# Kernel tuning notes

Hardware: AMD Instinct MI355X
Metric: run time of the kernel (lower is better)

## Reference

```python
import jax, jax.numpy as jnp
import numpy as np

NUM_HEADS = 8
EPS = 1e-3

N_TOKENS = 32768
DIM = 256
N_WIN = 128
WIN = N_TOKENS // N_WIN  # 256 tokens per window


def setup_inputs() -> dict:
    key = jax.random.key(0)
    ks = jax.random.split(key, 4)
    x = jax.random.normal(ks[0], (N_TOKENS, DIM), dtype=jnp.float32)
    # torch nn.Linear weights are [out_features, in_features]
    w_qkv = jax.random.normal(ks[1], (3 * DIM, DIM), dtype=jnp.float32) * (DIM ** -0.5)
    w_proj = jax.random.normal(ks[2], (DIM, DIM), dtype=jnp.float32) * (DIM ** -0.5)
    b_proj = jnp.zeros((DIM,), dtype=jnp.float32)
    batch_win_inds = (jnp.arange(N_TOKENS) // WIN).astype(jnp.int64)
    offsets = (jnp.arange(N_WIN) * WIN).astype(jnp.int64)
    counts = jnp.full((N_WIN,), WIN, dtype=jnp.int64)
    return {"x": x, "w_qkv": w_qkv, "w_proj": w_proj, "b_proj": b_proj,
            "offsets": offsets, "counts": counts, "batch_win_inds": batch_win_inds}


def reference(x, w_qkv, w_proj, b_proj, offsets, counts, batch_win_inds):
    N, C = x.shape
    H = NUM_HEADS
    hd = C // H
    W = counts.shape[0]  # number of windows (static)

    qkv = x @ w_qkv.T                      # [N, 3C]
    q, k, v = jnp.split(qkv, 3, axis=-1)   # each [N, C]
    q = jax.nn.relu(q.reshape(N, H, hd))   # [N, H, hd]
    k = jax.nn.relu(k.reshape(N, H, hd))
    v = v.reshape(N, H, hd)

    seg = batch_win_inds.astype(jnp.int32)
    # per-window KV state: kv[w] = sum_{i in w} k_i^T v_i   -> [W, H, hd, hd]
    kv = jax.ops.segment_sum(jnp.einsum('nhc,nhd->nhcd', k, v), seg, num_segments=W)
    # per-window key sum for normalizer                      -> [W, H, hd]
    s = jax.ops.segment_sum(k, seg, num_segments=W)

    y = jnp.einsum('nhc,nhcd->nhd', q, kv[seg])              # [N, H, hd]
    z = jnp.sum(s[seg] * q, axis=-1, keepdims=True)          # [N, H, 1]
    y = y / (z + EPS)

    y = y.reshape(N, C) @ w_proj.T + b_proj                  # [N, C]
    return y
```

## Files before the change

kernel.cpp:

```cpp
#include <hip/hip_runtime.h>

typedef __bf16 bf16_t;
typedef bf16_t bf16x8 __attribute__((ext_vector_type(8)));
typedef bf16_t bf16x4 __attribute__((ext_vector_type(4)));
typedef float f32x4 __attribute__((ext_vector_type(4)));

#define M_TOK 32768
#define NWIN 128
#define WIN  256

typedef __attribute__((address_space(3))) void* as3p;
typedef const __attribute__((address_space(1))) void* as1p;

__device__ __forceinline__ void gll16(const void* g, void* l) {
    __builtin_amdgcn_global_load_lds((as1p)g, (as3p)l, 16, 0, 0);
}

__device__ __forceinline__ bf16x8 cvt8(f32x4 a, f32x4 b) {
    bf16x8 o;
    o[0] = (bf16_t)a[0]; o[1] = (bf16_t)a[1]; o[2] = (bf16_t)a[2]; o[3] = (bf16_t)a[3];
    o[4] = (bf16_t)b[0]; o[5] = (bf16_t)b[1]; o[6] = (bf16_t)b[2]; o[7] = (bf16_t)b[3];
    return o;
}

#define VMW_(n) asm volatile("s_waitcnt vmcnt(" #n ")" ::: "memory")
#define VMW(n) VMW_(n)

__global__ __launch_bounds__(256) void wconv(
    const float* __restrict__ wq, const float* __restrict__ wp,
    bf16_t* __restrict__ wqb, bf16_t* __restrict__ wpb)
{
    int i4 = (blockIdx.x * 256 + threadIdx.x) * 4;
    const float* s; bf16_t* dst; int idx;
    if (i4 < 196608) { s = wq; dst = wqb; idx = i4; }
    else             { s = wp; dst = wpb; idx = i4 - 196608; }
    f32x4 v = *(const f32x4*)(s + idx);
    bf16x4 o;
    o[0] = (bf16_t)v[0]; o[1] = (bf16_t)v[1]; o[2] = (bf16_t)v[2]; o[3] = (bf16_t)v[3];
    *(bf16x4*)(dst + idx) = o;
}

__global__ __launch_bounds__(256) void gemm1_qkv(
    const float* __restrict__ X,
    const bf16_t* __restrict__ Wb,
    bf16_t* __restrict__ QKV)
{
    __shared__ __align__(16) float  As[3][128][32];
    __shared__ __align__(16) bf16_t Bs[3][128][32];

    const int tid = threadIdx.x;
    const int lane = tid & 63;
    const int wv = tid >> 6;
    const int wm = wv >> 1, wn = wv & 1;
    const int id = blockIdx.x;
    const int sg = id / 48, wsub = id % 48;
    const int m0 = (sg * 8 + (wsub & 7)) * 128;
    const int n0 = (wsub >> 3) * 128;
    const int r = lane & 15, q = lane >> 4;
    const int arow = lane >> 3;
    const int ag = (lane & 7) ^ arow;
    const int brow = lane >> 2;
    const int bg = (lane & 3) ^ (brow & 3);

    f32x4 acc[4][4] = {};

    auto stage = [&](int t, int buf) {
        const int kc = t * 32;
#pragma unroll
        for (int u = 0; u < 4; ++u) {
            const int rb = wv * 32 + u * 8;
            gll16(X + (size_t)(m0 + rb + arow) * 256 + kc + ag * 4, &As[buf][rb][0]);
        }
#pragma unroll
        for (int u = 0; u < 2; ++u) {
            const int rb = wv * 32 + u * 16;
            gll16(Wb + (size_t)(n0 + rb + brow) * 256 + kc + bg * 8, &Bs[buf][rb][0]);
        }
    };
    auto compute = [&](int buf) {
        bf16x8 a[4], b[4];
#pragma unroll
        for (int i = 0; i < 4; ++i) {
            const int row = wm * 64 + i * 16 + r;
            const int g0 = (2 * q) ^ (r & 7);
            const int g1 = (2 * q + 1) ^ (r & 7);
            f32x4 lo = *(const f32x4*)&As[buf][row][g0 * 4];
            f32x4 hi = *(const f32x4*)&As[buf][row][g1 * 4];
            a[i] = cvt8(lo, hi);
        }
#pragma unroll
        for (int j = 0; j < 4; ++j)
            b[j] = *(const bf16x8*)&Bs[buf][wn * 64 + j * 16 + r][(q ^ (r & 3)) * 8];
#pragma unroll
        for (int i = 0; i < 4; ++i)
#pragma unroll
            for (int j = 0; j < 4; ++j)
                acc[i][j] = __builtin_amdgcn_mfma_f32_16x16x32_bf16(b[j], a[i], acc[i][j], 0, 0, 0);
    };

    stage(0, 0); stage(1, 1); stage(2, 2);

#define G1_STEP(t, NW) do { \
        VMW(NW); \
        __builtin_amdgcn_s_barrier(); \
        __builtin_amdgcn_sched_barrier(0); \
        compute((t) % 3); \
        __builtin_amdgcn_sched_barrier(0); \
        __builtin_amdgcn_s_barrier(); \
        if ((t) + 3 < 8) stage((t) + 3, (t) % 3); \
    } while (0)

    G1_STEP(0, 12); G1_STEP(1, 12); G1_STEP(2, 12); G1_STEP(3, 12);
    G1_STEP(4, 12); G1_STEP(5, 12); G1_STEP(6, 6);  G1_STEP(7, 0);
#undef G1_STEP

#pragma unroll
    for (int i = 0; i < 4; ++i) {
        const int rowg = m0 + wm * 64 + i * 16 + r;
#pragma unroll
        for (int j = 0; j < 4; ++j) {
            const int nb = n0 + wn * 64 + j * 16 + q * 4;
            const int nblk = nb >> 5, d = nb & 31;
            bf16x4 o;
#pragma unroll
            for (int reg = 0; reg < 4; ++reg) {
                float v = acc[i][j][reg];
                if (nblk < 16) v = fmaxf(v, 0.0f);
                o[reg] = (bf16_t)v;
            }
            *(bf16x4*)&QKV[((size_t)nblk * M_TOK + rowg) * 32 + d] = o;
        }
    }
}

__global__ __launch_bounds__(256) void gemm2_proj(
    const bf16_t* __restrict__ Y,
    const bf16_t* __restrict__ Wb,
    const float* __restrict__ bias,
    float* __restrict__ Out)
{
    __shared__ __align__(16) bf16_t As[3][128][32];
    __shared__ __align__(16) bf16_t Bs[3][64][32];

    const int tid = threadIdx.x;
    const int lane = tid & 63;
    const int wv = tid >> 6;
    const int wm = wv >> 1, wn = wv & 1;
    const int id = blockIdx.x;
    const int sg = id / 32, wsub = id % 32;
    const int m0 = (sg * 8 + (wsub & 7)) * 128;
    const int n0 = (wsub >> 3) * 64;
    const int r = lane & 15, q = lane >> 4;
    const int brow = lane >> 2;
    const int bg = (lane & 3) ^ (brow & 3);

    f32x4 acc[4][2] = {};

    auto stage = [&](int t, int buf) {
        const int kc = t * 32;
#pragma unroll
        for (int u = 0; u < 2; ++u) {
            const int rb = wv * 32 + u * 16;
            gll16(Y + (size_t)(m0 + rb + brow) * 256 + kc + bg * 8, &As[buf][rb][0]);
        }
        gll16(Wb + (size_t)(n0 + wv * 16 + brow) * 256 + kc + bg * 8, &Bs[buf][wv * 16][0]);
    };
    auto compute = [&](int buf) {
        bf16x8 a[4], b[2];
#pragma unroll
        for (int i = 0; i < 4; ++i)
            a[i] = *(const bf16x8*)&As[buf][wm * 64 + i * 16 + r][(q ^ (r & 3)) * 8];
#pragma unroll
        for (int j = 0; j < 2; ++j)
            b[j] = *(const bf16x8*)&Bs[buf][wn * 32 + j * 16 + r][(q ^ (r & 3)) * 8];
#pragma unroll
        for (int i = 0; i < 4; ++i)
#pragma unroll
            for (int j = 0; j < 2; ++j)
                acc[i][j] = __builtin_amdgcn_mfma_f32_16x16x32_bf16(b[j], a[i], acc[i][j], 0, 0, 0);
    };

    stage(0, 0); stage(1, 1); stage(2, 2);

#define G2_STEP(t, NW) do { \
        VMW(NW); \
        __builtin_amdgcn_s_barrier(); \
        __builtin_amdgcn_sched_barrier(0); \
        compute((t) % 3); \
        __builtin_amdgcn_sched_barrier(0); \
        __builtin_amdgcn_s_barrier(); \
        if ((t) + 3 < 8) stage((t) + 3, (t) % 3); \
    } while (0)

    G2_STEP(0, 6); G2_STEP(1, 6); G2_STEP(2, 6); G2_STEP(3, 6);
    G2_STEP(4, 6); G2_STEP(5, 6); G2_STEP(6, 3); G2_STEP(7, 0);
#undef G2_STEP

#pragma unroll
    for (int i = 0; i < 4; ++i) {
        const int rowg = m0 + wm * 64 + i * 16 + r;
#pragma unroll
        for (int j = 0; j < 2; ++j) {
            const int nb = n0 + wn * 32 + j * 16 + q * 4;
            f32x4 bi = *(const f32x4*)(bias + nb);
            f32x4 o;
#pragma unroll
            for (int reg = 0; reg < 4; ++reg) o[reg] = acc[i][j][reg] + bi[reg];
            *(f32x4*)&Out[(size_t)rowg * 256 + nb] = o;
        }
    }
}

__global__ __launch_bounds__(256) void kvy_kernel(
    const bf16_t* __restrict__ QKV,
    const int* __restrict__ offsets,
    const int* __restrict__ counts,
    bf16_t* __restrict__ Y)
{
    const int w = blockIdx.x;
    const int h = blockIdx.y;
    const int is64 = (counts[1] == 0) ? 1 : 0;
    const int off = offsets[w << is64];
    const int tid = threadIdx.x;
    const int lane = tid & 63;
    const int wv = tid >> 6;

    __shared__ __align__(16) bf16_t KT[32 * 264];
    __shared__ __align__(16) bf16_t VT[32 * 264];
    __shared__ __align__(16) bf16_t KVT[32 * 40];
    __shared__ float sbuf[32];
    __shared__ float spart[32 * 8];
    __shared__ float zinv[WIN];

    {
        const int t = tid;
        const bf16_t* kp = QKV + ((size_t)(8 + h) * M_TOK + off + t) * 32;
        const bf16_t* vp = QKV + ((size_t)(16 + h) * M_TOK + off + t) * 32;
        bf16_t ka[32], va[32];
#pragma unroll
        for (int u = 0; u < 4; ++u) {
            bf16x8 kk = *(const bf16x8*)(kp + u * 8);
            bf16x8 vvv = *(const bf16x8*)(vp + u * 8);
#pragma unroll
            for (int j = 0; j < 8; ++j) { ka[u * 8 + j] = kk[j]; va[u * 8 + j] = vvv[j]; }
        }
#pragma unroll
        for (int c = 0; c < 32; ++c) {
            KT[c * 264 + t] = ka[c];
            VT[c * 264 + t] = va[c];
        }
    }
    __syncthreads();

    {
        const int c = tid >> 3;
        const int tc = (tid & 7) * 32;
        float ps = 0.f;
#pragma unroll
        for (int u = 0; u < 4; ++u) {
            bf16x8 kk = *(const bf16x8*)(&KT[c * 264 + tc + u * 8]);
#pragma unroll
            for (int j = 0; j < 8; ++j) ps += (float)kk[j];
        }
        spart[c * 8 + (tid & 7)] = ps;
    }
    {
        const int i = wv >> 1, j = wv & 1;
        const int r = lane & 15, q = lane >> 4;
        f32x4 acc = {};
#pragma unroll
        for (int ch = 0; ch < 8; ++ch) {
            bf16x8 af = *(const bf16x8*)(&KT[(i * 16 + r) * 264 + ch * 32 + q * 8]);
            bf16x8 bf_ = *(const bf16x8*)(&VT[(j * 16 + r) * 264 + ch * 32 + q * 8]);
            acc = __builtin_amdgcn_mfma_f32_16x16x32_bf16(af, bf_, acc, 0, 0, 0);
        }
        bf16x4 kv4;
#pragma unroll
        for (int reg = 0; reg < 4; ++reg) kv4[reg] = (bf16_t)acc[reg];
        *(bf16x4*)(&KVT[(j * 16 + r) * 40 + i * 16 + q * 4]) = kv4;
    }
    __syncthreads();
    if (tid < 32) {
        float s = 0.f;
#pragma unroll
        for (int u = 0; u < 8; ++u) s += spart[tid * 8 + u];
        sbuf[tid] = s;
    }
    __syncthreads();

    {
        const int t = tid;
        const bf16_t* qp = QKV + ((size_t)h * M_TOK + off + t) * 32;
        float z = 0.f;
#pragma unroll
        for (int u = 0; u < 4; ++u) {
            bf16x8 qq = *(const bf16x8*)(qp + u * 8);
#pragma unroll
            for (int j = 0; j < 8; ++j) z += (float)qq[j] * sbuf[u * 8 + j];
        }
        zinv[t] = 1.0f / (z + 1e-3f);
    }
    __syncthreads();

    {
        const int r = lane & 15, q = lane >> 4;
        bf16x8 b0 = *(const bf16x8*)(&KVT[(r) * 40 + q * 8]);
        bf16x8 b1 = *(const bf16x8*)(&KVT[(16 + r) * 40 + q * 8]);
#pragma unroll
        for (int u = 0; u < 4; ++u) {
            const int mi = wv * 4 + u;
            const bf16_t* ap = QKV + ((size_t)h * M_TOK + off + mi * 16 + r) * 32 + q * 8;
            bf16x8 af = *(const bf16x8*)ap;
            f32x4 acc0 = {}, acc1 = {};
            acc0 = __builtin_amdgcn_mfma_f32_16x16x32_bf16(b0, af, acc0, 0, 0, 0);
            acc1 = __builtin_amdgcn_mfma_f32_16x16x32_bf16(b1, af, acc1, 0, 0, 0);
            const int tkn = mi * 16 + r;
            const float zi = zinv[tkn];
            bf16_t* yp = Y + (size_t)(off + tkn) * 256 + h * 32;
            bf16x4 o0, o1;
#pragma unroll
            for (int reg = 0; reg < 4; ++reg) {
                o0[reg] = (bf16_t)(acc0[reg] * zi);
                o1[reg] = (bf16_t)(acc1[reg] * zi);
            }
            *(bf16x4*)(yp + q * 4) = o0;
            *(bf16x4*)(yp + 16 + q * 4) = o1;
        }
    }
}

extern "C" void kernel_launch(void* const* d_in, const int* in_sizes, int n_in,
                              void* d_out, int out_size, void* d_ws, size_t ws_size,
                              hipStream_t stream) {
    const float* x      = (const float*)d_in[0];
    const float* w_qkv  = (const float*)d_in[1];
    const float* w_proj = (const float*)d_in[2];
    const float* b_proj = (const float*)d_in[3];
    const int*   offs   = (const int*)d_in[4];
    const int*   cnts   = (const int*)d_in[5];

    char* ws = (char*)d_ws;
    bf16_t* QKV = (bf16_t*)ws;
    bf16_t* Y   = (bf16_t*)(ws + 50331648);
    bf16_t* Wqb = (bf16_t*)(ws + 67108864);
    bf16_t* Wpb = (bf16_t*)(ws + 67502080);
    float*  out = (float*)d_out;

    wconv<<<256, 256, 0, stream>>>(w_qkv, w_proj, Wqb, Wpb);

    gemm1_qkv<<<1536, 256, 0, stream>>>(x, Wqb, QKV);

    kvy_kernel<<<dim3(NWIN, 8), 256, 0, stream>>>(QKV, offs, cnts, Y);

    gemm2_proj<<<1024, 256, 0, stream>>>(Y, Wpb, b_proj, out);
}
```

Baseline: 145.4 us.

## Keep full-K A row block resident in LDS and sweep all N tiles per block

Both GEMMs now give each 512-thread block a 128-row slab of A that is loaded once into LDS in bf16 (converted from fp32 in gemm1, copied directly in gemm2). The block then loops over all output column tiles, streaming weight tiles through a triple buffer. This removes the repeated reads of X that the old grid made, once per N-tile, and the repeated per-tile fp32 to bf16 conversion. The cost is a much smaller grid of 256 blocks, lower occupancy from the large LDS footprint, and a serial initial A load that is not overlapped with compute in gemm1.

```diff
diff --git a/kernel.cpp b/kernel.cpp
--- a/kernel.cpp
+++ b/kernel.cpp
@@ -40,175 +40,197 @@
     *(bf16x4*)(dst + idx) = o;
 }
 
-__global__ __launch_bounds__(256) void gemm1_qkv(
+__global__ __launch_bounds__(512) void gemm1_qkv(
     const float* __restrict__ X,
     const bf16_t* __restrict__ Wb,
     bf16_t* __restrict__ QKV)
 {
-    __shared__ __align__(16) float  As[3][128][32];
-    __shared__ __align__(16) bf16_t Bs[3][128][32];
+    __shared__ __align__(16) bf16_t Al[128][256];
+    __shared__ __align__(16) bf16_t Bs[3][128][64];
 
     const int tid = threadIdx.x;
     const int lane = tid & 63;
     const int wv = tid >> 6;
-    const int wm = wv >> 1, wn = wv & 1;
-    const int id = blockIdx.x;
-    const int sg = id / 48, wsub = id % 48;
-    const int m0 = (sg * 8 + (wsub & 7)) * 128;
-    const int n0 = (wsub >> 3) * 128;
+    const int wm = wv >> 2, wn = wv & 3;
+    const int m0 = blockIdx.x * 128;
     const int r = lane & 15, q = lane >> 4;
-    const int arow = lane >> 3;
-    const int ag = (lane & 7) ^ arow;
-    const int brow = lane >> 2;
-    const int bg = (lane & 3) ^ (brow & 3);
-
-    f32x4 acc[4][4] = {};
-
-    auto stage = [&](int t, int buf) {
-        const int kc = t * 32;
-#pragma unroll
-        for (int u = 0; u < 4; ++u) {
-            const int rb = wv * 32 + u * 8;
-            gll16(X + (size_t)(m0 + rb + arow) * 256 + kc + ag * 4, &As[buf][rb][0]);
-        }
-#pragma unroll
-        for (int u = 0; u < 2; ++u) {
-            const int rb = wv * 32 + u * 16;
-            gll16(Wb + (size_t)(n0 + rb + brow) * 256 + kc + bg * 8, &Bs[buf][rb][0]);
-        }
-    };
-    auto compute = [&](int buf) {
-        bf16x8 a[4], b[4];
+    const int rl = lane >> 3, gsl = lane & 7;
+
+    f32x4 acc[4][2] = {};
+
+    auto stageB = [&](int t) {
+        const int nb = t >> 2, kc = (t & 3) * 64;
+#pragma unroll
+        for (int u = 0; u < 2; ++u)
+            gll16(Wb + (size_t)(nb * 128 + wv * 16 + u * 8 + rl) * 256 + kc + (gsl ^ rl) * 8,
+                  &Bs[t % 3][wv * 16 + u * 8][0]);
+    };
+
+    auto comp = [&](int t) {
+        const int buf = t % 3;
+#pragma unroll
+        for (int s = 0; s < 2; ++s) {
+            const int kk = (t & 3) * 2 + s;
+            bf16x8 a[4], b[2];
+#pragma unroll
+            for (int i = 0; i < 4; ++i)
+                a[i] = *(const bf16x8*)((const bf16_t*)Al +
+                        (wm * 64 + i * 16 + r) * 256 + ((kk * 4 + q) ^ (r & 7)) * 8);
+#pragma unroll
+            for (int j = 0; j < 2; ++j)
+                b[j] = *(const bf16x8*)&Bs[buf][wn * 32 + j * 16 + r][((s * 4 + q) ^ (r & 7)) * 8];
+#pragma unroll
+            for (int i = 0; i < 4; ++i)
+#pragma unroll
+                for (int j = 0; j < 2; ++j)
+                    acc[i][j] = __builtin_amdgcn_mfma_f32_16x16x32_bf16(b[j], a[i], acc[i][j], 0, 0, 0);
+        }
+    };
+
+    auto wout = [&](int nb) {
 #pragma unroll
         for (int i = 0; i < 4; ++i) {
-            const int row = wm * 64 + i * 16 + r;
-            const int g0 = (2 * q) ^ (r & 7);
-            const int g1 = (2 * q + 1) ^ (r & 7);
-            f32x4 lo = *(const f32x4*)&As[buf][row][g0 * 4];
-            f32x4 hi = *(const f32x4*)&As[buf][row][g1 * 4];
-            a[i] = cvt8(lo, hi);
-        }
-#pragma unroll
-        for (int j = 0; j < 4; ++j)
-            b[j] = *(const bf16x8*)&Bs[buf][wn * 64 + j * 16 + r][(q ^ (r & 3)) * 8];
-#pragma unroll
-        for (int i = 0; i < 4; ++i)
-#pragma unroll
-            for (int j = 0; j < 4; ++j)
-                acc[i][j] = __builtin_amdgcn_mfma_f32_16x16x32_bf16(b[j], a[i], acc[i][j], 0, 0, 0);
-    };
-
-    stage(0, 0); stage(1, 1); stage(2, 2);
-
-#define G1_STEP(t, NW) do { \
+            const int rowg = m0 + wm * 64 + i * 16 + r;
+#pragma unroll
+            for (int j = 0; j < 2; ++j) {
+                const int nbcol = nb * 128 + wn * 32 + j * 16 + q * 4;
+                const int nblk = nbcol >> 5, d = nbcol & 31;
+                bf16x4 o;
+#pragma unroll
+                for (int reg = 0; reg < 4; ++reg) {
+                    float v = acc[i][j][reg];
+                    if (nblk < 16) v = fmaxf(v, 0.0f);
+                    o[reg] = (bf16_t)v;
+                }
+                *(bf16x4*)&QKV[((size_t)nblk * M_TOK + rowg) * 32 + d] = o;
+                acc[i][j] = (f32x4){0.f, 0.f, 0.f, 0.f};
+            }
+        }
+    };
+
+    stageB(0); stageB(1); stageB(2);
+
+#pragma unroll
+    for (int it = 0; it < 16; ++it) {
+        const int L = it * 512 + tid;
+        const int row = L >> 6, col4 = L & 63;
+        f32x4 v = *(const f32x4*)(X + (size_t)(m0 + row) * 256 + col4 * 4);
+        bf16x4 o;
+        o[0] = (bf16_t)v[0]; o[1] = (bf16_t)v[1]; o[2] = (bf16_t)v[2]; o[3] = (bf16_t)v[3];
+        const int gs = (col4 >> 1) ^ (row & 7);
+        *(bf16x4*)((bf16_t*)Al + row * 256 + gs * 8 + (col4 & 1) * 4) = o;
+    }
+    __syncthreads();
+
+#define G1S(t, NW) do { \
         VMW(NW); \
         __builtin_amdgcn_s_barrier(); \
         __builtin_amdgcn_sched_barrier(0); \
-        compute((t) % 3); \
+        comp(t); \
+        if (((t) & 3) == 3) wout((t) >> 2); \
         __builtin_amdgcn_sched_barrier(0); \
         __builtin_amdgcn_s_barrier(); \
-        if ((t) + 3 < 8) stage((t) + 3, (t) % 3); \
+        if ((t) + 3 < 24) stageB((t) + 3); \
     } while (0)
 
-    G1_STEP(0, 12); G1_STEP(1, 12); G1_STEP(2, 12); G1_STEP(3, 12);
-    G1_STEP(4, 12); G1_STEP(5, 12); G1_STEP(6, 6);  G1_STEP(7, 0);
-#undef G1_STEP
-
-#pragma unroll
-    for (int i = 0; i < 4; ++i) {
-        const int rowg = m0 + wm * 64 + i * 16 + r;
-#pragma unroll
-        for (int j = 0; j < 4; ++j) {
-            const int nb = n0 + wn * 64 + j * 16 + q * 4;
-            const int nblk = nb >> 5, d = nb & 31;
-            bf16x4 o;
-#pragma unroll
-            for (int reg = 0; reg < 4; ++reg) {
-                float v = acc[i][j][reg];
-                if (nblk < 16) v = fmaxf(v, 0.0f);
-                o[reg] = (bf16_t)v;
-            }
-            *(bf16x4*)&QKV[((size_t)nblk * M_TOK + rowg) * 32 + d] = o;
-        }
-    }
-}
-
-__global__ __launch_bounds__(256) void gemm2_proj(
+    G1S(0, 4);  G1S(1, 4);  G1S(2, 4);  G1S(3, 4);
+    G1S(4, 4);  G1S(5, 4);  G1S(6, 4);  G1S(7, 4);
+    G1S(8, 4);  G1S(9, 4);  G1S(10, 4); G1S(11, 4);
+    G1S(12, 4); G1S(13, 4); G1S(14, 4); G1S(15, 4);
+    G1S(16, 4); G1S(17, 4); G1S(18, 4); G1S(19, 4);
+    G1S(20, 4); G1S(21, 4); G1S(22, 2); G1S(23, 0);
+#undef G1S
+}
+
+__global__ __launch_bounds__(512) void gemm2_proj(
     const bf16_t* __restrict__ Y,
     const bf16_t* __restrict__ Wb,
     const float* __restrict__ bias,
     float* __restrict__ Out)
 {
-    __shared__ __align__(16) bf16_t As[3][128][32];
-    __shared__ __align__(16) bf16_t Bs[3][64][32];
+    __shared__ __align__(16) bf16_t Al[128][256];
+    __shared__ __align__(16) bf16_t Bs[3][128][64];
 
     const int tid = threadIdx.x;
     const int lane = tid & 63;
     const int wv = tid >> 6;
-    const int wm = wv >> 1, wn = wv & 1;
-    const int id = blockIdx.x;
-    const int sg = id / 32, wsub = id % 32;
-    const int m0 = (sg * 8 + (wsub & 7)) * 128;
-    const int n0 = (wsub >> 3) * 64;
+    const int wm = wv >> 2, wn = wv & 3;
+    const int m0 = blockIdx.x * 128;
     const int r = lane & 15, q = lane >> 4;
-    const int brow = lane >> 2;
-    const int bg = (lane & 3) ^ (brow & 3);
+    const int rl = lane >> 3, gsl = lane & 7;
 
     f32x4 acc[4][2] = {};
 
-    auto stage = [&](int t, int buf) {
-        const int kc = t * 32;
-#pragma unroll
-        for (int u = 0; u < 2; ++u) {
-            const int rb = wv * 32 + u * 16;
-            gll16(Y + (size_t)(m0 + rb + brow) * 256 + kc + bg * 8, &As[buf][rb][0]);
-        }
-        gll16(Wb + (size_t)(n0 + wv * 16 + brow) * 256 + kc + bg * 8, &Bs[buf][wv * 16][0]);
-    };
-    auto compute = [&](int buf) {
-        bf16x8 a[4], b[2];
-#pragma unroll
-        for (int i = 0; i < 4; ++i)
-            a[i] = *(const bf16x8*)&As[buf][wm * 64 + i * 16 + r][(q ^ (r & 3)) * 8];
-#pragma unroll
-        for (int j = 0; j < 2; ++j)
-            b[j] = *(const bf16x8*)&Bs[buf][wn * 32 + j * 16 + r][(q ^ (r & 3)) * 8];
-#pragma unroll
-        for (int i = 0; i < 4; ++i)
+    auto stageB = [&](int t) {
+        const int nb = t >> 2, kc = (t & 3) * 64;
+#pragma unroll
+        for (int u = 0; u < 2; ++u)
+            gll16(Wb + (size_t)(nb * 128 + wv * 16 + u * 8 + rl) * 256 + kc + (gsl ^ rl) * 8,
+                  &Bs[t % 3][wv * 16 + u * 8][0]);
+    };
+
+    auto comp = [&](int t) {
+        const int buf = t % 3;
+#pragma unroll
+        for (int s = 0; s < 2; ++s) {
+            const int kk = (t & 3) * 2 + s;
+            bf16x8 a[4], b[2];
+#pragma unroll
+            for (int i = 0; i < 4; ++i)
+                a[i] = *(const bf16x8*)((const bf16_t*)Al +
+                        (wm * 64 + i * 16 + r) * 256 + ((kk * 4 + q) ^ (r & 7)) * 8);
 #pragma unroll
             for (int j = 0; j < 2; ++j)
-                acc[i][j] = __builtin_amdgcn_mfma_f32_16x16x32_bf16(b[j], a[i], acc[i][j], 0, 0, 0);
-    };
-
-    stage(0, 0); stage(1, 1); stage(2, 2);
-
-#define G2_STEP(t, NW) do { \
+                b[j] = *(const bf16x8*)&Bs[buf][wn * 32 + j * 16 + r][((s * 4 + q) ^ (r & 7)) * 8];
+#pragma unroll
+            for (int i = 0; i < 4; ++i)
+#pragma unroll
+                for (int j = 0; j < 2; ++j)
+                    acc[i][j] = __builtin_amdgcn_mfma_f32_16x16x32_bf16(b[j], a[i], acc[i][j], 0, 0, 0);
+        }
+    };
+
+    auto wout = [&](int nb) {
+#pragma unroll
+        for (int i = 0; i < 4; ++i) {
+            const int rowg = m0 + wm * 64 + i * 16 + r;
+#pragma unroll
+            for (int j = 0; j < 2; ++j) {
+                const int n = nb * 128 + wn * 32 + j * 16 + q * 4;
+                f32x4 bi = *(const f32x4*)(bias + n);
+                f32x4 o;
+#pragma unroll
+                for (int reg = 0; reg < 4; ++reg) o[reg] = acc[i][j][reg] + bi[reg];
+                *(f32x4*)&Out[(size_t)rowg * 256 + n] = o;
+                acc[i][j] = (f32x4){0.f, 0.f, 0.f, 0.f};
+            }
+        }
+    };
+
+    {
+#pragma unroll
+        for (int u = 0; u < 8; ++u) {
+            const int rowl = wv * 16 + u * 2 + (lane >> 5);
+            const int gsrc = (lane & 31) ^ (rowl & 7);
+            gll16(Y + (size_t)(m0 + rowl) * 256 + gsrc * 8, &Al[wv * 16 + u * 2][0]);
+        }
+    }
+    stageB(0); stageB(1); stageB(2);
+
+#define G2S(t, NW) do { \
         VMW(NW); \
         __builtin_amdgcn_s_barrier(); \
         __builtin_amdgcn_sched_barrier(0); \
-        compute((t) % 3); \
+        comp(t); \
+        if (((t) & 3) == 3) wout((t) >> 2); \
         __builtin_amdgcn_sched_barrier(0); \
         __builtin_amdgcn_s_barrier(); \
-        if ((t) + 3 < 8) stage((t) + 3, (t) % 3); \
+        if ((t) + 3 < 8) stageB((t) + 3); \
     } while (0)
 
-    G2_STEP(0, 6); G2_STEP(1, 6); G2_STEP(2, 6); G2_STEP(3, 6);
-    G2_STEP(4, 6); G2_STEP(5, 6); G2_STEP(6, 3); G2_STEP(7, 0);
-#undef G2_STEP
-
-#pragma unroll
-    for (int i = 0; i < 4; ++i) {
-        const int rowg = m0 + wm * 64 + i * 16 + r;
-#pragma unroll
-        for (int j = 0; j < 2; ++j) {
-            const int nb = n0 + wn * 32 + j * 16 + q * 4;
-            f32x4 bi = *(const f32x4*)(bias + nb);
-            f32x4 o;
-#pragma unroll
-            for (int reg = 0; reg < 4; ++reg) o[reg] = acc[i][j][reg] + bi[reg];
-            *(f32x4*)&Out[(size_t)rowg * 256 + nb] = o;
-        }
-    }
+    G2S(0, 4); G2S(1, 4); G2S(2, 4); G2S(3, 4);
+    G2S(4, 4); G2S(5, 4); G2S(6, 2); G2S(7, 0);
+#undef G2S
 }
 
 __global__ __launch_bounds__(256) void kvy_kernel(
@@ -348,9 +370,9 @@
 
     wconv<<<256, 256, 0, stream>>>(w_qkv, w_proj, Wqb, Wpb);
 
-    gemm1_qkv<<<1536, 256, 0, stream>>>(x, Wqb, QKV);
+    gemm1_qkv<<<256, 512, 0, stream>>>(x, Wqb, QKV);
 
     kvy_kernel<<<dim3(NWIN, 8), 256, 0, stream>>>(QKV, offs, cnts, Y);
 
-    gemm2_proj<<<1024, 256, 0, stream>>>(Y, Wpb, b_proj, out);
-}
+    gemm2_proj<<<256, 512, 0, stream>>>(Y, Wpb, b_proj, out);
+}
```

Result: faster. 141.6 us (-2.6%).
